# Kernel tuning notes

Hardware: AMD Instinct MI355X
Metric: run time of the kernel (lower is better)

Reference implementation:

```python
import jax, jax.numpy as jnp
import numpy as np

B, F, D = 16384, 32, 64
EPS = 1e-5


def layer_norm(x, g, b):
    m = x.mean(-1, keepdims=True)
    v = ((x - m) ** 2).mean(-1, keepdims=True)
    return (x - m) / jnp.sqrt(v + EPS) * g + b


def setup_inputs() -> dict:
    key = jax.random.key(0)
    ks = jax.random.split(key, 24)
    IN = F * D

    def w(k, shape, fan_in):
        return jax.random.normal(k, shape, dtype=jnp.float32) / np.sqrt(fan_in)

    return {
        "x": jax.random.normal(ks[0], (B, F, D), dtype=jnp.float32),
        # StaticGRN (mask branch): Linear(IN,D) -> ELU -> Linear(D,F); skip Linear(IN,F); GateAndNorm(F)
        "mw1": w(ks[1], (IN, D), IN), "mb1": jnp.zeros((D,), jnp.float32),
        "mw2": w(ks[2], (D, F), D), "mb2": jnp.zeros((F,), jnp.float32),
        "mlw": w(ks[3], (IN, F), IN), "mlb": jnp.zeros((F,), jnp.float32),
        "mgw": w(ks[4], (F, F), F), "mgb": jnp.zeros((F,), jnp.float32),
        "mlw2": w(ks[5], (F, F), F), "mlb2": jnp.zeros((F,), jnp.float32),
        "mgamma": jnp.ones((F,), jnp.float32), "mbeta": jnp.zeros((F,), jnp.float32),
        # Per-feature GRNNoContext params, stacked over F (batched small GEMMs)
        "w1": w(ks[6], (F, D, D), D), "b1": jnp.zeros((F, D), jnp.float32),
        "w2": w(ks[7], (F, D, D), D), "b2": jnp.zeros((F, D), jnp.float32),
        "gw": w(ks[8], (F, D, D), D), "gb": jnp.zeros((F, D), jnp.float32),
        "lw": w(ks[9], (F, D, D), D), "lb": jnp.zeros((F, D), jnp.float32),
        "gamma": jnp.ones((F, D), jnp.float32), "beta": jnp.zeros((F, D), jnp.float32),
    }


def reference(x, mw1, mb1, mw2, mb2, mlw, mlb, mgw, mgb, mlw2, mlb2, mgamma, mbeta,
              w1, b1, w2, b2, gw, gb, lw, lb, gamma, beta):
    b, f, d = x.shape
    flat = x.reshape(b, f * d)
    # StaticGRN mask branch (dropout is 0.0 -> identity)
    h = jax.nn.elu(flat @ mw1 + mb1) @ mw2 + mb2          # [B,F]
    res = flat @ mlw + mlb                                 # [B,F] skip path
    pre = jax.nn.sigmoid(h @ mgw + mgb) * (h @ mlw2 + mlb2) + res
    mask = jax.nn.softmax(layer_norm(pre, mgamma, mbeta), axis=-1)[:, None, :]  # [B,1,F]
    # Per-feature GRNs, batched over the feature axis
    hh = jax.nn.elu(jnp.einsum('bfd,fde->bfe', x, w1) + b1)
    hh = jnp.einsum('bfd,fde->bfe', hh, w2) + b2
    gate = jax.nn.sigmoid(jnp.einsum('bfd,fde->bfe', hh, gw) + gb)
    lin = jnp.einsum('bfd,fde->bfe', hh, lw) + lb
    vecs = layer_norm(gate * lin + x, gamma, beta)         # [B,F,D]
    out = jnp.einsum('bof,bfd->bod', mask, vecs)[:, 0, :]  # [B,D]
    return out, mask
```

## Files before the change

### kernel.cpp

```cpp
#include <hip/hip_runtime.h>
#include <math.h>

#define NB 16384
#define NF 32
#define ND 64
#define NIN 2048

typedef __attribute__((ext_vector_type(8))) short fragA;
typedef __attribute__((ext_vector_type(4))) float fragC;

#define MFMA(a, b, c) __builtin_amdgcn_mfma_f32_16x16x32_bf16((a), (b), (c), 0, 0, 0)

__device__ __forceinline__ short f2bf(float f) {
    union { float f; unsigned u; } v; v.f = f;
    return (short)((v.u + 0x7fffu + ((v.u >> 16) & 1u)) >> 16);
}
__device__ __forceinline__ fragA cvt8(const float* p) {
    float4 a = *(const float4*)p;
    float4 b = *(const float4*)(p + 4);
    fragA r;
    r[0] = f2bf(a.x); r[1] = f2bf(a.y); r[2] = f2bf(a.z); r[3] = f2bf(a.w);
    r[4] = f2bf(b.x); r[5] = f2bf(b.y); r[6] = f2bf(b.z); r[7] = f2bf(b.w);
    return r;
}

__global__ __launch_bounds__(256) void prep_kernel(
    const float* __restrict__ w1, const float* __restrict__ w2,
    const float* __restrict__ gw, const float* __restrict__ lw,
    const float* __restrict__ mw1, const float* __restrict__ mlw,
    short* __restrict__ wsout)
{
    int F = blockIdx.x * 256 + threadIdx.x;
    fragA o;
    if (F < 65536) {
        int mat = F >> 14;
        int f   = (F >> 9) & 31;
        int nt  = (F >> 7) & 3;
        int s   = (F >> 6) & 1;
        int l   = F & 63;
        const float* src = (mat == 0 ? w1 : mat == 1 ? w2 : mat == 2 ? gw : lw)
                           + (size_t)f * 4096;
        int n  = nt * 16 + (l & 15);
        int k0 = s * 32 + ((l >> 4) << 3);
#pragma unroll
        for (int j = 0; j < 8; ++j) o[j] = f2bf(src[(k0 + j) * 64 + n]);
    } else {
        int G  = F - 65536;
        int f  = G / 768;
        int r  = G - f * 768;
        int nt = r >> 7;
        int s  = (r >> 6) & 1;
        int l  = r & 63;
        int n  = nt * 16 + (l & 15);
        int k0 = f * 64 + s * 32 + ((l >> 4) << 3);
        if (n < 64) {
#pragma unroll
            for (int j = 0; j < 8; ++j) o[j] = f2bf(mw1[(size_t)(k0 + j) * 64 + n]);
        } else {
#pragma unroll
            for (int j = 0; j < 8; ++j) o[j] = f2bf(mlw[(size_t)(k0 + j) * 32 + (n - 64)]);
        }
    }
    ((fragA*)wsout)[F] = o;
}

__global__ __launch_bounds__(256, 3) void fused_kernel(
    const float* __restrict__ x,
    const short* __restrict__ wfrag, const short* __restrict__ mwfrag,
    const float* __restrict__ mb1, const float* __restrict__ mw2,
    const float* __restrict__ mb2, const float* __restrict__ mlb,
    const float* __restrict__ mgw, const float* __restrict__ mgb,
    const float* __restrict__ mlw2, const float* __restrict__ mlb2,
    const float* __restrict__ mgamma, const float* __restrict__ mbeta,
    const float* __restrict__ b1, const float* __restrict__ b2,
    const float* __restrict__ gb, const float* __restrict__ lb,
    const float* __restrict__ gamma, const float* __restrict__ beta,
    float* __restrict__ mask_out, float* __restrict__ out)
{
    __shared__ float smem[12992];
    float* redS  = smem;
    float* wmw2  = smem + 6208;
    float* wmgw  = smem + 8512;
    float* wmlw2 = smem + 9664;
    float* hS1   = smem + 10816;
    float* resS  = smem + 11904;
    float* maskS = smem + 12480;
    float* h2S   = smem;
    float* preS  = smem + 640;

    const int tid = threadIdx.x;
    const int w = tid >> 6, l = tid & 63;
    const int row0 = blockIdx.x * 16;
    const int m = l & 15, q = l >> 4;

    const fragA* wf  = (const fragA*)wfrag;
    const fragA* mwf = (const fragA*)mwfrag;

    fragC acc[6];
#pragma unroll
    for (int nt = 0; nt < 6; ++nt) acc[nt] = (fragC){0.f, 0.f, 0.f, 0.f};

    const float* xpm = x + (size_t)(row0 + m) * NIN + q * 8;
    for (int fi = 0; fi < 8; ++fi) {
        int f = w * 8 + fi;
        const float* xp = xpm + f * ND;
        fragA a0 = cvt8(xp), a1 = cvt8(xp + 32);
        const size_t fb = (size_t)f * 768 + l;
#pragma unroll
        for (int nt = 0; nt < 6; ++nt) {
            acc[nt] = MFMA(a0, mwf[fb + nt * 128], acc[nt]);
            acc[nt] = MFMA(a1, mwf[fb + nt * 128 + 64], acc[nt]);
        }
    }
#pragma unroll
    for (int nt = 0; nt < 6; ++nt)
#pragma unroll
        for (int rg = 0; rg < 4; ++rg)
            redS[w * 1552 + (q * 4 + rg) * 97 + nt * 16 + m] = acc[nt][rg];
    for (int i = tid; i < 2048; i += 256) wmw2[(i >> 5) * 36 + (i & 31)] = mw2[i];
    for (int i = tid; i < 1024; i += 256) {
        wmgw[(i >> 5) * 36 + (i & 31)]  = mgw[i];
        wmlw2[(i >> 5) * 36 + (i & 31)] = mlw2[i];
    }
    __syncthreads();

    {
        int r = tid & 15, cb = tid >> 4;
#pragma unroll
        for (int i = 0; i < 6; ++i) {
            int c = cb + i * 16;
            float s = redS[r * 97 + c] + redS[1552 + r * 97 + c]
                    + redS[3104 + r * 97 + c] + redS[4656 + r * 97 + c];
            if (c < 64) {
                float v = s + mb1[c];
                hS1[r * 68 + c] = v > 0.f ? v : expm1f(v);
            } else {
                resS[r * 36 + (c - 64)] = s + mlb[c - 64];
            }
        }
    }
    __syncthreads();

    {
        int r = tid & 15, c = tid >> 4;
        float h0 = mb2[c], h1 = mb2[c + 16];
        for (int k = 0; k < 64; ++k) {
            float hv = hS1[r * 68 + k];
            h0 += hv * wmw2[k * 36 + c];
            h1 += hv * wmw2[k * 36 + c + 16];
        }
        h2S[r * 36 + c] = h0;
        h2S[r * 36 + c + 16] = h1;
    }
    __syncthreads();

    {
        int r = tid & 15, c = tid >> 4;
        float g0 = mgb[c], g1 = mgb[c + 16], l0 = mlb2[c], l1 = mlb2[c + 16];
        for (int k = 0; k < 32; ++k) {
            float hv = h2S[r * 36 + k];
            g0 += hv * wmgw[k * 36 + c];
            g1 += hv * wmgw[k * 36 + c + 16];
            l0 += hv * wmlw2[k * 36 + c];
            l1 += hv * wmlw2[k * 36 + c + 16];
        }
        preS[r * 36 + c]      = l0 / (1.f + expf(-g0)) + resS[r * 36 + c];
        preS[r * 36 + c + 16] = l1 / (1.f + expf(-g1)) + resS[r * 36 + c + 16];
    }
    __syncthreads();

    if (w == 0) {
        int r2 = l >> 2, c0 = (l & 3) * 8;
        float pre[8];
#pragma unroll
        for (int i = 0; i < 8; ++i) pre[i] = preS[r2 * 36 + c0 + i];
        float s1 = 0.f;
#pragma unroll
        for (int i = 0; i < 8; ++i) s1 += pre[i];
        s1 += __shfl_xor(s1, 1); s1 += __shfl_xor(s1, 2);
        float mean = s1 * (1.f / 32.f);
        float s2 = 0.f;
#pragma unroll
        for (int i = 0; i < 8; ++i) { float d = pre[i] - mean; s2 += d * d; }
        s2 += __shfl_xor(s2, 1); s2 += __shfl_xor(s2, 2);
        float inv = rsqrtf(s2 * (1.f / 32.f) + 1e-5f);
        float ln[8]; float mx = -3.4e38f;
#pragma unroll
        for (int i = 0; i < 8; ++i) {
            ln[i] = (pre[i] - mean) * inv * mgamma[c0 + i] + mbeta[c0 + i];
            mx = fmaxf(mx, ln[i]);
        }
        mx = fmaxf(mx, __shfl_xor(mx, 1));
        mx = fmaxf(mx, __shfl_xor(mx, 2));
        float ssum = 0.f;
#pragma unroll
        for (int i = 0; i < 8; ++i) { ln[i] = expf(ln[i] - mx); ssum += ln[i]; }
        ssum += __shfl_xor(ssum, 1); ssum += __shfl_xor(ssum, 2);
        float rs = 1.f / ssum;
        float* mo = mask_out + (size_t)(row0 + r2) * 32 + c0;
        *(float4*)mo       = (float4){ln[0] * rs, ln[1] * rs, ln[2] * rs, ln[3] * rs};
        *(float4*)(mo + 4) = (float4){ln[4] * rs, ln[5] * rs, ln[6] * rs, ln[7] * rs};
#pragma unroll
        for (int i = 0; i < 8; ++i) maskS[r2 * 32 + c0 + i] = ln[i] * rs;
    }
    __syncthreads();

    float* hW   = smem + w * 1088;
    float* outS = smem + 4352;

    fragC oac[4];
#pragma unroll
    for (int nt = 0; nt < 4; ++nt) oac[nt] = (fragC){0.f, 0.f, 0.f, 0.f};

    for (int fi = 0; fi < 8; ++fi) {
        int f = w * 8 + fi;
        float xres[4][4];
#pragma unroll
        for (int rg = 0; rg < 4; ++rg)
#pragma unroll
            for (int nt = 0; nt < 4; ++nt)
                xres[rg][nt] = x[(size_t)(row0 + q * 4 + rg) * NIN + f * ND + nt * 16 + m];
        float b1v[4], b2v[4], gbv[4], lbv[4], gmv[4], btv[4];
#pragma unroll
        for (int nt = 0; nt < 4; ++nt) {
            int c = f * 64 + nt * 16 + m;
            b1v[nt] = b1[c]; b2v[nt] = b2[c]; gbv[nt] = gb[c];
            lbv[nt] = lb[c]; gmv[nt] = gamma[c]; btv[nt] = beta[c];
        }
        float mk[4];
#pragma unroll
        for (int rg = 0; rg < 4; ++rg) mk[rg] = maskS[(q * 4 + rg) * 32 + f];

        {
            const float* xp = xpm + f * ND;
            fragA a0 = cvt8(xp), a1 = cvt8(xp + 32);
            const size_t base = (size_t)f * 512 + l;
#pragma unroll
            for (int nt = 0; nt < 4; ++nt) {
                fragC c = {0.f, 0.f, 0.f, 0.f};
                c = MFMA(a0, wf[base + nt * 128], c);
                c = MFMA(a1, wf[base + nt * 128 + 64], c);
                int col = nt * 16 + m;
#pragma unroll
                for (int rg = 0; rg < 4; ++rg) {
                    float v = c[rg] + b1v[nt];
                    hW[(q * 4 + rg) * 68 + col] = v > 0.f ? v : expm1f(v);
                }
            }
        }
        {
            const float* ap = hW + m * 68 + q * 8;
            fragA a0 = cvt8(ap), a1 = cvt8(ap + 32);
            const size_t base = ((size_t)(NF + f)) * 512 + l;
            fragC cc[4];
#pragma unroll
            for (int nt = 0; nt < 4; ++nt) {
                fragC c = {0.f, 0.f, 0.f, 0.f};
                c = MFMA(a0, wf[base + nt * 128], c);
                c = MFMA(a1, wf[base + nt * 128 + 64], c);
                cc[nt] = c;
            }
#pragma unroll
            for (int nt = 0; nt < 4; ++nt) {
                int col = nt * 16 + m;
#pragma unroll
                for (int rg = 0; rg < 4; ++rg)
                    hW[(q * 4 + rg) * 68 + col] = cc[nt][rg] + b2v[nt];
            }
        }
        {
            const float* ap = hW + m * 68 + q * 8;
            fragA a0 = cvt8(ap), a1 = cvt8(ap + 32);
            const size_t baseg = ((size_t)(2 * NF + f)) * 512 + l;
            const size_t basel = ((size_t)(3 * NF + f)) * 512 + l;
            fragC ga[4], la[4];
#pragma unroll
            for (int nt = 0; nt < 4; ++nt) {
                fragC g = {0.f, 0.f, 0.f, 0.f}, li = {0.f, 0.f, 0.f, 0.f};
                g  = MFMA(a0, wf[baseg + nt * 128], g);
                g  = MFMA(a1, wf[baseg + nt * 128 + 64], g);
                li = MFMA(a0, wf[basel + nt * 128], li);
                li = MFMA(a1, wf[basel + nt * 128 + 64], li);
                ga[nt] = g; la[nt] = li;
            }
#pragma unroll
            for (int rg = 0; rg < 4; ++rg) {
                float val[4];
#pragma unroll
                for (int nt = 0; nt < 4; ++nt) {
                    float gg = ga[nt][rg] + gbv[nt];
                    float ll = la[nt][rg] + lbv[nt];
                    val[nt] = ll / (1.f + expf(-gg)) + xres[rg][nt];
                }
                float s1 = val[0] + val[1] + val[2] + val[3];
                s1 += __shfl_xor(s1, 1); s1 += __shfl_xor(s1, 2);
                s1 += __shfl_xor(s1, 4); s1 += __shfl_xor(s1, 8);
                float mean = s1 * (1.f / 64.f);
                float s2 = 0.f;
#pragma unroll
                for (int nt = 0; nt < 4; ++nt) { float d = val[nt] - mean; s2 += d * d; }
                s2 += __shfl_xor(s2, 1); s2 += __shfl_xor(s2, 2);
                s2 += __shfl_xor(s2, 4); s2 += __shfl_xor(s2, 8);
                float inv = rsqrtf(s2 * (1.f / 64.f) + 1e-5f);
#pragma unroll
                for (int nt = 0; nt < 4; ++nt) {
                    float vec = (val[nt] - mean) * inv * gmv[nt] + btv[nt];
                    oac[nt][rg] += mk[rg] * vec;
                }
            }
        }
    }

#pragma unroll
    for (int nt = 0; nt < 4; ++nt)
#pragma unroll
        for (int rg = 0; rg < 4; ++rg)
            outS[w * 1088 + (q * 4 + rg) * 68 + nt * 16 + m] = oac[nt][rg];
    __syncthreads();
    {
        int t4 = tid * 4;
        int r = t4 >> 6, c = t4 & 63;
        float v[4];
#pragma unroll
        for (int j = 0; j < 4; ++j) {
            v[j] = outS[r * 68 + c + j] + outS[1088 + r * 68 + c + j]
                 + outS[2176 + r * 68 + c + j] + outS[3264 + r * 68 + c + j];
        }
        *(float4*)(out + (size_t)(row0 + r) * 64 + c) = (float4){v[0], v[1], v[2], v[3]};
    }
}

extern "C" void kernel_launch(void* const* d_in, const int* in_sizes, int n_in,
                              void* d_out, int out_size, void* d_ws, size_t ws_size,
                              hipStream_t stream) {
    const float* x      = (const float*)d_in[0];
    const float* mw1    = (const float*)d_in[1];
    const float* mb1    = (const float*)d_in[2];
    const float* mw2    = (const float*)d_in[3];
    const float* mb2    = (const float*)d_in[4];
    const float* mlw    = (const float*)d_in[5];
    const float* mlb    = (const float*)d_in[6];
    const float* mgw    = (const float*)d_in[7];
    const float* mgb    = (const float*)d_in[8];
    const float* mlw2   = (const float*)d_in[9];
    const float* mlb2   = (const float*)d_in[10];
    const float* mgamma = (const float*)d_in[11];
    const float* mbeta  = (const float*)d_in[12];
    const float* w1     = (const float*)d_in[13];
    const float* b1     = (const float*)d_in[14];
    const float* w2     = (const float*)d_in[15];
    const float* b2     = (const float*)d_in[16];
    const float* gw     = (const float*)d_in[17];
    const float* gb     = (const float*)d_in[18];
    const float* lw     = (const float*)d_in[19];
    const float* lb     = (const float*)d_in[20];
    const float* gamma  = (const float*)d_in[21];
    const float* beta   = (const float*)d_in[22];

    float* out  = (float*)d_out;
    float* mask = out + (size_t)NB * 64;

    short* wfrag  = (short*)d_ws;
    short* mwfrag = wfrag + (size_t)65536 * 8;

    hipLaunchKernelGGL(prep_kernel, dim3(352), dim3(256), 0, stream,
                       w1, w2, gw, lw, mw1, mlw, wfrag);
    hipLaunchKernelGGL(fused_kernel, dim3(NB / 16), dim3(256), 0, stream,
                       x, wfrag, mwfrag,
                       mb1, mw2, mb2, mlb, mgw, mgb, mlw2, mlb2, mgamma, mbeta,
                       b1, b2, gb, lb, gamma, beta,
                       mask, out);
}
```

Before: 363.3 us.

## Shrink LDS footprint with atomic reduction to raise occupancy to four blocks

Replaces the four per-wave partial-sum buffers for the mask-branch GEMM with a single zero-initialised buffer reduced through LDS atomicAdd. The smaller buffer, plus dropping row padding on several shared arrays and repacking the shared layout, cuts LDS per block so the launch bound can request four blocks per CU instead of three. It also switches the bf16 conversion to the packed HIP intrinsic. In exchange it adds LDS atomics and an extra barrier for zeroing, removes padding that may have avoided bank conflicts, and tightens the register budget.

Measured after the change: 357.7 us. Within noise of the previous version (-1.5%).

```diff
diff --git a/kernel.cpp b/kernel.cpp
--- a/kernel.cpp
+++ b/kernel.cpp
@@ -1,4 +1,5 @@
 #include <hip/hip_runtime.h>
+#include <hip/hip_bf16.h>
 #include <math.h>
 
 #define NB 16384
@@ -16,12 +17,14 @@
     return (short)((v.u + 0x7fffu + ((v.u >> 16) & 1u)) >> 16);
 }
 __device__ __forceinline__ fragA cvt8(const float* p) {
-    float4 a = *(const float4*)p;
-    float4 b = *(const float4*)(p + 4);
-    fragA r;
-    r[0] = f2bf(a.x); r[1] = f2bf(a.y); r[2] = f2bf(a.z); r[3] = f2bf(a.w);
-    r[4] = f2bf(b.x); r[5] = f2bf(b.y); r[6] = f2bf(b.z); r[7] = f2bf(b.w);
-    return r;
+    const float4 a = *(const float4*)p;
+    const float4 b = *(const float4*)(p + 4);
+    union { __hip_bfloat162 h[4]; fragA f; } u;
+    u.h[0] = __float22bfloat162_rn(make_float2(a.x, a.y));
+    u.h[1] = __float22bfloat162_rn(make_float2(a.z, a.w));
+    u.h[2] = __float22bfloat162_rn(make_float2(b.x, b.y));
+    u.h[3] = __float22bfloat162_rn(make_float2(b.z, b.w));
+    return u.f;
 }
 
 __global__ __launch_bounds__(256) void prep_kernel(
@@ -64,7 +67,7 @@
     ((fragA*)wsout)[F] = o;
 }
 
-__global__ __launch_bounds__(256, 3) void fused_kernel(
+__global__ __launch_bounds__(256, 4) void fused_kernel(
     const float* __restrict__ x,
     const short* __restrict__ wfrag, const short* __restrict__ mwfrag,
     const float* __restrict__ mb1, const float* __restrict__ mw2,
@@ -77,16 +80,17 @@
     const float* __restrict__ gamma, const float* __restrict__ beta,
     float* __restrict__ mask_out, float* __restrict__ out)
 {
-    __shared__ float smem[12992];
+    __shared__ float smem[8960];
     float* redS  = smem;
-    float* wmw2  = smem + 6208;
-    float* wmgw  = smem + 8512;
-    float* wmlw2 = smem + 9664;
-    float* hS1   = smem + 10816;
-    float* resS  = smem + 11904;
-    float* maskS = smem + 12480;
-    float* h2S   = smem;
-    float* preS  = smem + 640;
+    float* wmw2  = smem + 1552;
+    float* wmgw  = smem + 3600;
+    float* wmlw2 = smem + 4624;
+    float* hS1   = smem + 5648;
+    float* resS  = smem + 6736;
+    float* h2S   = smem + 7312;
+    float* preS  = smem;
+    float* maskS = smem + 8448;
+    float* outS  = smem + 4352;
 
     const int tid = threadIdx.x;
     const int w = tid >> 6, l = tid & 63;
@@ -95,6 +99,9 @@
 
     const fragA* wf  = (const fragA*)wfrag;
     const fragA* mwf = (const fragA*)mwfrag;
+
+    for (int i = tid; i < 1552; i += 256) redS[i] = 0.f;
+    __syncthreads();
 
     fragC acc[6];
 #pragma unroll
@@ -112,16 +119,16 @@
             acc[nt] = MFMA(a1, mwf[fb + nt * 128 + 64], acc[nt]);
         }
     }
+    for (int i = tid; i < 2048; i += 256) wmw2[i] = mw2[i];
+    for (int i = tid; i < 1024; i += 256) {
+        wmgw[i]  = mgw[i];
+        wmlw2[i] = mlw2[i];
+    }
 #pragma unroll
     for (int nt = 0; nt < 6; ++nt)
 #pragma unroll
         for (int rg = 0; rg < 4; ++rg)
-            redS[w * 1552 + (q * 4 + rg) * 97 + nt * 16 + m] = acc[nt][rg];
-    for (int i = tid; i < 2048; i += 256) wmw2[(i >> 5) * 36 + (i & 31)] = mw2[i];
-    for (int i = tid; i < 1024; i += 256) {
-        wmgw[(i >> 5) * 36 + (i & 31)]  = mgw[i];
-        wmlw2[(i >> 5) * 36 + (i & 31)] = mlw2[i];
-    }
+            atomicAdd(&redS[(q * 4 + rg) * 97 + nt * 16 + m], acc[nt][rg]);
     __syncthreads();
 
     {
@@ -129,8 +136,7 @@
 #pragma unroll
         for (int i = 0; i < 6; ++i) {
             int c = cb + i * 16;
-            float s = redS[r * 97 + c] + redS[1552 + r * 97 + c]
-                    + redS[3104 + r * 97 + c] + redS[4656 + r * 97 + c];
+            float s = redS[r * 97 + c];
             if (c < 64) {
                 float v = s + mb1[c];
                 hS1[r * 68 + c] = v > 0.f ? v : expm1f(v);
@@ -146,8 +152,8 @@
         float h0 = mb2[c], h1 = mb2[c + 16];
         for (int k = 0; k < 64; ++k) {
             float hv = hS1[r * 68 + k];
-            h0 += hv * wmw2[k * 36 + c];
-            h1 += hv * wmw2[k * 36 + c + 16];
+            h0 += hv * wmw2[k * 32 + c];
+            h1 += hv * wmw2[k * 32 + c + 16];
         }
         h2S[r * 36 + c] = h0;
         h2S[r * 36 + c + 16] = h1;
@@ -159,10 +165,10 @@
         float g0 = mgb[c], g1 = mgb[c + 16], l0 = mlb2[c], l1 = mlb2[c + 16];
         for (int k = 0; k < 32; ++k) {
             float hv = h2S[r * 36 + k];
-            g0 += hv * wmgw[k * 36 + c];
-            g1 += hv * wmgw[k * 36 + c + 16];
-            l0 += hv * wmlw2[k * 36 + c];
-            l1 += hv * wmlw2[k * 36 + c + 16];
+            g0 += hv * wmgw[k * 32 + c];
+            g1 += hv * wmgw[k * 32 + c + 16];
+            l0 += hv * wmlw2[k * 32 + c];
+            l1 += hv * wmlw2[k * 32 + c + 16];
         }
         preS[r * 36 + c]      = l0 / (1.f + expf(-g0)) + resS[r * 36 + c];
         preS[r * 36 + c + 16] = l1 / (1.f + expf(-g1)) + resS[r * 36 + c + 16];
@@ -205,8 +211,7 @@
     }
     __syncthreads();
 
-    float* hW   = smem + w * 1088;
-    float* outS = smem + 4352;
+    float* hW = smem + w * 1088;
 
     fragC oac[4];
 #pragma unroll
@@ -315,7 +320,7 @@
     for (int nt = 0; nt < 4; ++nt)
 #pragma unroll
         for (int rg = 0; rg < 4; ++rg)
-            outS[w * 1088 + (q * 4 + rg) * 68 + nt * 16 + m] = oac[nt][rg];
+            outS[w * 1024 + (q * 4 + rg) * 64 + nt * 16 + m] = oac[nt][rg];
     __syncthreads();
     {
         int t4 = tid * 4;
@@ -323,8 +328,8 @@
         float v[4];
 #pragma unroll
         for (int j = 0; j < 4; ++j) {
-            v[j] = outS[r * 68 + c + j] + outS[1088 + r * 68 + c + j]
-                 + outS[2176 + r * 68 + c + j] + outS[3264 + r * 68 + c + j];
+            v[j] = outS[r * 64 + c + j] + outS[1024 + r * 64 + c + j]
+                 + outS[2048 + r * 64 + c + j] + outS[3072 + r * 64 + c + j];
         }
         *(float4*)(out + (size_t)(row0 + r) * 64 + c) = (float4){v[0], v[1], v[2], v[3]};
     }
```
